# Kernel optimization log

Hardware: AMD Instinct MI355X
Metric: run time of the kernel (lower is better)

The kernel has to match this reference:

```python
import jax, jax.numpy as jnp
import numpy as np

KS = 3   # kernel_size
PAD = 1  # padding
N_K = KS * KS


def conv2d(x, w, b=None, stride=1, pad=0):
    out = jax.lax.conv_general_dilated(
        x, w, (stride, stride), [(pad, pad), (pad, pad)],
        dimension_numbers=('NCHW', 'OIHW', 'NCHW'))
    if b is not None:
        out = out + b[None, :, None, None]
    return out


def deform_sample(x, offset):
    # x: [b,c,H,W]  offset: [b,2N,h,w] -> [b,c,h,w,N]
    b, c, H, W = x.shape
    _, twoN, h, w = offset.shape
    N = twoN // 2
    xp = jnp.pad(x, ((0, 0), (0, 0), (PAD, PAD), (PAD, PAD)))
    Hp, Wp = H + 2 * PAD, W + 2 * PAD
    r = (KS - 1) // 2
    knx, kny = jnp.meshgrid(jnp.arange(-r, r + 1), jnp.arange(-r, r + 1), indexing='ij')
    pnx = knx.reshape(-1).astype(offset.dtype)  # [N] kernel x offsets
    pny = kny.reshape(-1).astype(offset.dtype)
    off = jnp.transpose(offset, (0, 2, 3, 1))   # [b,h,w,2N]
    p0x = (jnp.arange(h) + PAD).astype(offset.dtype)
    p0y = (jnp.arange(w) + PAD).astype(offset.dtype)
    px = p0x[None, :, None, None] + pnx[None, None, None, :] + off[..., :N]  # [b,h,w,N]
    py = p0y[None, None, :, None] + pny[None, None, None, :] + off[..., N:]
    # q = p.detach().floor() in torch -> stop_gradient here
    flx = jnp.floor(jax.lax.stop_gradient(px))
    fly = jnp.floor(jax.lax.stop_gradient(py))
    qltx = jnp.clip(flx, 0, Hp - 1)
    qrbx = jnp.clip(flx + 1, 0, Hp - 1)
    qlty = jnp.clip(fly, 0, Wp - 1)
    qrby = jnp.clip(fly + 1, 0, Wp - 1)
    pxc = jnp.clip(px, 0, Hp - 1)
    pyc = jnp.clip(py, 0, Wp - 1)
    g_lt = (1 + (qltx - pxc)) * (1 + (qlty - pyc))
    g_rb = (1 - (qrbx - pxc)) * (1 - (qrby - pyc))
    g_lb = (1 - (qrbx - pxc)) * (1 + (qlty - pyc))
    g_rt = (1 + (qltx - pxc)) * (1 - (qrby - pyc))
    ix_lt, ix_rb = qltx.astype(jnp.int32), qrbx.astype(jnp.int32)
    iy_lt, iy_rb = qlty.astype(jnp.int32), qrby.astype(jnp.int32)

    def gather(ix, iy):
        def one(xb, ixb, iyb):
            return xb[:, ixb, iyb]  # [c,h,w,N]
        return jax.vmap(one)(xp, ix, iy)

    x_lt = gather(ix_lt, iy_lt)
    x_rb = gather(ix_rb, iy_rb)
    x_lb = gather(ix_rb, iy_lt)
    x_rt = gather(ix_lt, iy_rb)
    return (g_lt[:, None] * x_lt + g_rb[:, None] * x_rb
            + g_lb[:, None] * x_lb + g_rt[:, None] * x_rt)


def z_weight(z, mode):
    # cubic interpolation basis weights; z: [b,N,h,w] -> [b,1,h,w,N]
    if mode == '1':
        w = 1 - 11.0 / 6.0 * z + z ** 2 - 1.0 / 6.0 * z ** 3
    elif mode == '2':
        w = 3 * z - 2.5 * z ** 2 + 0.5 * z ** 3
    elif mode == '4':
        w = -1.5 * z + 2 * z ** 2 - 0.5 * z ** 3
    else:
        w = 1.0 / 3.0 * z - 0.5 * z ** 2 + 1.0 / 6.0 * z ** 3
    return jnp.transpose(w, (0, 2, 3, 1))[:, None]


def reshape_x_offset(xo):
    # [b,c,h,w,ks*ks] -> [b,c,h*ks,w*ks] (torch cat/view equivalent)
    b, c, h, w, _ = xo.shape
    xo = xo.reshape(b, c, h, w, KS, KS)          # N = g*ks + k
    xo = jnp.transpose(xo, (0, 1, 2, 4, 3, 5))   # (b,c,h,g,w,k)
    return xo.reshape(b, c, h * KS, w * KS)


def setup_inputs() -> dict:
    key = jax.random.key(0)
    ks = jax.random.split(key, 18)
    B, C, OSC, OUTC, H, W = 2, 64, 64, 64, 128, 128
    f = jax.random.normal
    inp = {
        'img1': f(ks[0], (B, C, H, W), jnp.float32),
        'img2': f(ks[1], (B, C, H, W), jnp.float32),
        'img4': f(ks[2], (B, C, H, W), jnp.float32),
        'img5': f(ks[3], (B, C, H, W), jnp.float32),
        'offset_source': f(ks[4], (B, OSC, H, W), jnp.float32),
        'w_pc1': f(ks[5], (2 * N_K, OSC, 5, 5), jnp.float32) * 0.01,
        'b_pc1': f(ks[6], (2 * N_K,), jnp.float32) * 0.01,
        'w_pc2': f(ks[7], (2 * N_K, OSC, 5, 5), jnp.float32) * 0.01,
        'b_pc2': f(ks[8], (2 * N_K,), jnp.float32) * 0.01,
        'w_pc4': f(ks[9], (2 * N_K, OSC, 5, 5), jnp.float32) * 0.01,
        'b_pc4': f(ks[10], (2 * N_K,), jnp.float32) * 0.01,
        'w_pc5': f(ks[11], (2 * N_K, OSC, 5, 5), jnp.float32) * 0.01,
        'b_pc5': f(ks[12], (2 * N_K,), jnp.float32) * 0.01,
        'w_z': f(ks[13], (N_K, OSC, 5, 5), jnp.float32) * 0.01,
        'b_z': f(ks[14], (N_K,), jnp.float32) * 0.01,
        'w_m': f(ks[15], (N_K, OSC, 5, 5), jnp.float32) * 0.01,
        'b_m': f(ks[16], (N_K,), jnp.float32) * 0.01,
        'w_conv': f(ks[17], (OUTC, C, KS, KS), jnp.float32) * 0.05,
    }
    return inp


def reference(img1, img2, img4, img5, offset_source,
              w_pc1, b_pc1, w_pc2, b_pc2, w_pc4, b_pc4, w_pc5, b_pc5,
              w_z, b_z, w_m, b_m, w_conv):
    off1 = conv2d(offset_source, w_pc1, b_pc1, pad=2)
    off2 = conv2d(offset_source, w_pc2, b_pc2, pad=2)
    off4 = conv2d(offset_source, w_pc4, b_pc4, pad=2)
    off5 = conv2d(offset_source, w_pc5, b_pc5, pad=2)
    z = 3.0 * jax.nn.sigmoid(conv2d(offset_source, w_z, b_z, pad=2))
    m = jax.nn.sigmoid(conv2d(offset_source, w_m, b_m, pad=2))
    f1 = deform_sample(img1, off1)
    f2 = deform_sample(img2, off2)
    f4 = deform_sample(img4, off4)
    f5 = deform_sample(img5, off5)
    central = (f1 * z_weight(z, '1') + f2 * z_weight(z, '2')
               + f4 * z_weight(z, '4') + f5 * z_weight(z, '5'))
    central = central * jnp.transpose(m, (0, 2, 3, 1))[:, None]
    out = conv2d(reshape_x_offset(central), w_conv, None, stride=KS)
    return out
```

## Files before the change

kernel.cpp:

```cpp
#include <hip/hip_runtime.h>
#include <hip/hip_bf16.h>
#include <math.h>

#define HWX 16384

typedef __attribute__((ext_vector_type(8))) short short8v;
typedef __attribute__((ext_vector_type(4))) float f32x4;

__device__ inline ushort f2bf(float x) {
    union { __hip_bfloat16 h; ushort u; } cv;
    cv.h = __float2bfloat16(x);
    return cv.u;
}

__global__ __launch_bounds__(256) void packw_kernel(
    const float* __restrict__ w1, const float* __restrict__ b1,
    const float* __restrict__ w2, const float* __restrict__ b2,
    const float* __restrict__ w4, const float* __restrict__ b4,
    const float* __restrict__ w5, const float* __restrict__ b5,
    const float* __restrict__ wz, const float* __restrict__ bz,
    const float* __restrict__ wm, const float* __restrict__ bm,
    __hip_bfloat16* __restrict__ Wpk, float* __restrict__ bpack)
{
    const int idx = blockIdx.x * 256 + threadIdx.x;
    if (idx < 96) {
        const int o = idx; float v = 0.f;
        if      (o < 18) v = b1[o];
        else if (o < 36) v = b2[o - 18];
        else if (o < 54) v = b4[o - 36];
        else if (o < 72) v = b5[o - 54];
        else if (o < 81) v = bz[o - 72];
        else if (o < 90) v = bm[o - 81];
        bpack[o] = v;
    }
    if (idx < 96 * 1600) {
        const int o   = idx / 1600;
        const int k   = idx - o * 1600;
        const int kyx = k >> 6;
        const int ic  = k & 63;
        const int off = ic * 25 + kyx;
        float v = 0.f;
        if      (o < 18) v = w1[o * 1600 + off];
        else if (o < 36) v = w2[(o - 18) * 1600 + off];
        else if (o < 54) v = w4[(o - 36) * 1600 + off];
        else if (o < 72) v = w5[(o - 54) * 1600 + off];
        else if (o < 81) v = wz[(o - 72) * 1600 + off];
        else if (o < 90) v = wm[(o - 81) * 1600 + off];
        Wpk[idx] = __float2bfloat16(v);
    }
}

__global__ __launch_bounds__(256) void packosT_kernel(
    const float* __restrict__ src, __hip_bfloat16* __restrict__ osT)
{
    const int yy = blockIdx.x;
    const int b  = blockIdx.y;
    __hip_bfloat16* dst = osT + ((size_t)b * 132 + yy) * 132 * 64;
    for (int idx = threadIdx.x; idx < 132 * 64; idx += 256) {
        const int xx = idx >> 6;
        const int c  = idx & 63;
        float v = 0.f;
        if (yy >= 2 && yy < 130 && xx >= 2 && xx < 130)
            v = src[(((b << 6) + c) << 14) + ((yy - 2) << 7) + (xx - 2)];
        dst[idx] = __float2bfloat16(v);
    }
}

__global__ __launch_bounds__(256) void conv_mfma_kernel(
    const __hip_bfloat16* __restrict__ Wpk,
    const float* __restrict__ bpack,
    const __hip_bfloat16* __restrict__ osT,
    float* __restrict__ offs,
    float* __restrict__ zbuf,
    float* __restrict__ mbuf)
{
    __shared__ __align__(16) ushort slab[5 * 68 * 64];
    __shared__ __align__(16) ushort wbuf[2][96 * 64];

    const int bx = blockIdx.x;
    const int y  = bx >> 1;
    const int x0 = (bx & 1) << 6;
    const int b  = blockIdx.y;
    const int t    = threadIdx.x;
    const int wv   = t >> 6;
    const int lane = t & 63;
    const int l15  = lane & 15;
    const int kgrp = lane >> 4;
    const int wm   = wv >> 1;
    const int wn   = wv & 1;

    const ushort* ob = (const ushort*)osT + (size_t)b * (132 * 132 * 64);
    const ushort* Wg = (const ushort*)Wpk;

    for (int c = t; c < 2720; c += 256) {
        const int r5  = c / 544;
        const int rem = c - r5 * 544;
        const int col = rem >> 3;
        const int cb  = rem & 7;
        const short8v v = *(const short8v*)(ob + (((y + r5) * 132 + x0 + col) << 6) + (cb << 3));
        const int slot = r5 * 544 + (col << 3) + (cb ^ (col & 7));
        *(short8v*)((char*)slab + slot * 16) = v;
    }

#define STAGE_W(kyx, bi)                                                       \
    _Pragma("unroll")                                                          \
    for (int it = 0; it < 3; ++it) {                                           \
        const int c  = it * 256 + t;                                           \
        const int oc = c >> 3, cb = c & 7;                                     \
        const ushort* src = Wg + oc * 1600 + (kyx) * 64 + ((cb ^ (oc & 7)) << 3); \
        __builtin_amdgcn_global_load_lds(                                      \
            (const __attribute__((address_space(1))) void*)src,                \
            (__attribute__((address_space(3))) void*)((char*)wbuf[bi] + (it * 256 + wv * 64) * 16), \
            16, 0, 0);                                                         \
    }

    STAGE_W(0, 0)
    __syncthreads();

    f32x4 acc[3][2];
    #pragma unroll
    for (int m = 0; m < 3; ++m)
        #pragma unroll
        for (int n = 0; n < 2; ++n) acc[m][n] = (f32x4){0.f, 0.f, 0.f, 0.f};

    for (int kyx = 0; kyx < 25; ++kyx) {
        const int bi = kyx & 1;
        if (kyx < 24) STAGE_W(kyx + 1, bi ^ 1)
        const int ky = kyx / 5, kx = kyx % 5;
        #pragma unroll
        for (int kc = 0; kc < 2; ++kc) {
            const int kcg = (kc << 2) + kgrp;
            short8v af[3], bf[2];
            #pragma unroll
            for (int m = 0; m < 3; ++m) {
                const int oc = wm * 48 + m * 16 + l15;
                af[m] = *(const short8v*)((char*)wbuf[bi] + ((oc << 3) + (kcg ^ (oc & 7))) * 16);
            }
            #pragma unroll
            for (int n = 0; n < 2; ++n) {
                const int col = wn * 32 + n * 16 + l15 + kx;
                bf[n] = *(const short8v*)((char*)slab + ((ky * 68 + col) * 8 + (kcg ^ (col & 7))) * 16);
            }
            #pragma unroll
            for (int m = 0; m < 3; ++m)
                #pragma unroll
                for (int n = 0; n < 2; ++n)
                    acc[m][n] = __builtin_amdgcn_mfma_f32_16x16x32_bf16(af[m], bf[n], acc[m][n], 0, 0, 0);
        }
        __syncthreads();
    }
#undef STAGE_W

    #pragma unroll
    for (int m = 0; m < 3; ++m) {
        const int ocb = wm * 48 + m * 16 + (kgrp << 2);
        #pragma unroll
        for (int n = 0; n < 2; ++n) {
            const int x = x0 + wn * 32 + n * 16 + l15;
            const int p = (y << 7) + x;
            #pragma unroll
            for (int r = 0; r < 4; ++r) {
                const int o = ocb + r;
                const float v = acc[m][n][r] + bpack[o];
                if (o < 72) {
                    const int i = o / 18, ch = o - i * 18;
                    offs[i * (2 * 18 * HWX) + (((b * 18) + ch) << 14) + p] = v;
                } else if (o < 81) {
                    zbuf[((b * 9 + (o - 72)) << 14) + p] = 3.f / (1.f + expf(-v));
                } else if (o < 90) {
                    mbuf[((b * 9 + (o - 81)) << 14) + p] = 1.f / (1.f + expf(-v));
                }
            }
        }
    }
}

__global__ __launch_bounds__(256) void transpose_kernel(
    const float* __restrict__ i0, const float* __restrict__ i1,
    const float* __restrict__ i2, const float* __restrict__ i3,
    ushort* __restrict__ imgT)
{
    const int img = blockIdx.z;
    const int b   = blockIdx.y;
    const int p0  = blockIdx.x << 6;
    const float* src = (img == 0) ? i0 : (img == 1) ? i1 : (img == 2) ? i2 : i3;

    __shared__ float tile[64][65];
    const int t = threadIdx.x;
    const int pp = t & 63, c0 = t >> 6;
    #pragma unroll
    for (int k = 0; k < 16; ++k) {
        const int c = (k << 2) + c0;
        tile[c][pp] = src[(((b << 6) + c) << 14) + p0 + pp];
    }
    __syncthreads();
    const int c2 = t & 31, pl = t >> 5;
    #pragma unroll
    for (int k = 0; k < 8; ++k) {
        const int pi = (k << 3) + pl;
        const uint packed = (uint)f2bf(tile[2 * c2][pi])
                          | ((uint)f2bf(tile[2 * c2 + 1][pi]) << 16);
        *(uint*)(imgT + ((size_t)(((img << 1) + b) << 14) + p0 + pi) * 64 + 2 * c2)
            = packed;
    }
}

__global__ __launch_bounds__(256) void wcpk_kernel(
    const float* __restrict__ wc, __hip_bfloat16* __restrict__ WcPk)
{
    const int idx = blockIdx.x * 256 + threadIdx.x;
    if (idx < 36864) WcPk[idx] = __float2bfloat16(wc[idx]);
}

__global__ __launch_bounds__(256, 5) void fused_kernel(
    const float* __restrict__ offs,
    const float* __restrict__ zbuf,
    const float* __restrict__ mbuf,
    const ushort* __restrict__ imgT,
    const __hip_bfloat16* __restrict__ WcPk,
    float* __restrict__ out)
{
    __shared__ __hip_bfloat16 s_sb[16 * 584];
    __shared__ ushort4 s_ti[16 * 36];
    __shared__ float4  s_tw4[16 * 36];

    const int t   = threadIdx.x;
    const int pid = blockIdx.x;
    const int b   = pid >> 10;
    const int rem = pid & 1023;
    const int h   = rem >> 3;
    const int w0p = (rem & 7) << 4;

    for (int u = t; u < 576; u += 256) {
        const int px   = u / 36;
        const int unit = u - px * 36;
        const int i    = unit / 9;
        const int n    = unit - i * 9;
        const int wcol = w0p + px;
        const int p    = (h << 7) + wcol;

        const float* ob = offs + i * (2 * 18 * HWX) + ((b * 18) << 14);
        const float ox = ob[(n << 14) + p];
        const float oy = ob[((n + 9) << 14) + p];
        const float z  = zbuf[((b * 9 + n) << 14) + p];
        const float mm = mbuf[((b * 9 + n) << 14) + p];

        const float zc0 = (i == 0) ? 1.f : 0.f;
        const float zc1 = (i == 0) ? (-11.f / 6.f) : (i == 1) ? 3.f
                         : (i == 2) ? -1.5f : (1.f / 3.f);
        const float zc2 = (i == 0) ? 1.f : (i == 1) ? -2.5f
                         : (i == 2) ? 2.f : -0.5f;
        const float zc3 = (i == 0) ? (-1.f / 6.f) : (i == 1) ? 0.5f
                         : (i == 2) ? -0.5f : (1.f / 6.f);
        const float zw   = zc0 + z * (zc1 + z * (zc2 + z * zc3));
        const float coef = zw * mm;

        const float pxf = (float)(h + n / 3) + ox;
        const float pyf = (float)(wcol + n % 3) + oy;
        const float flx = floorf(pxf), fly = floorf(pyf);
        const float qltx = fminf(fmaxf(flx, 0.f), 129.f);
        const float qrbx = fminf(fmaxf(flx + 1.f, 0.f), 129.f);
        const float qlty = fminf(fmaxf(fly, 0.f), 129.f);
        const float qrby = fminf(fmaxf(fly + 1.f, 0.f), 129.f);
        const float pxc = fminf(fmaxf(pxf, 0.f), 129.f);
        const float pyc = fminf(fmaxf(pyf, 0.f), 129.f);
        const float gxl = 1.f + (qltx - pxc);
        const float gxr = 1.f - (qrbx - pxc);
        const float gyl = 1.f + (qlty - pyc);
        const float gyr = 1.f - (qrby - pyc);
        const int ixl = (int)qltx, ixr = (int)qrbx;
        const int iyl = (int)qlty, iyr = (int)qrby;

        ushort4 ti; float4 tw;
        auto mk = [&](int qx, int qy, float g, ushort& ii, float& ww) {
            const bool valid = (qx >= 1) && (qx <= 128) && (qy >= 1) && (qy <= 128);
            ii = (ushort)(valid ? (((qx - 1) << 7) + (qy - 1)) : 0);
            ww = valid ? g * coef : 0.f;
        };
        mk(ixl, iyl, gxl * gyl, ti.x, tw.x);
        mk(ixr, iyr, gxr * gyr, ti.y, tw.y);
        mk(ixr, iyl, gxr * gyl, ti.z, tw.z);
        mk(ixl, iyr, gxl * gyr, ti.w, tw.w);
        s_ti[u]  = ti;
        s_tw4[u] = tw;
    }
    __syncthreads();

    const int lane = t & 63;
    const int wv   = t >> 6;
    const int c4   = lane & 15;
    const int pxs  = lane >> 4;
    const int px   = (wv << 2) + pxs;

    f32x4 s4[9];
    #pragma unroll
    for (int n = 0; n < 9; ++n) s4[n] = (f32x4){0.f, 0.f, 0.f, 0.f};

    const int tb = px * 36;
    #pragma unroll 1
    for (int i = 0; i < 4; ++i) {
        const char* ibl = (const char*)(imgT + (((size_t)((i << 1) + b)) << 20)) + (c4 << 3);
        #pragma unroll
        for (int n = 0; n < 9; ++n) {
            const ushort4 tib = s_ti[tb + i * 9 + n];
            const float4  tw  = s_tw4[tb + i * 9 + n];
            {
                const uint2 v = *(const uint2*)(ibl + ((uint)tib.x << 7));
                s4[n].x = fmaf(tw.x, __uint_as_float(v.x << 16),         s4[n].x);
                s4[n].y = fmaf(tw.x, __uint_as_float(v.x & 0xffff0000u), s4[n].y);
                s4[n].z = fmaf(tw.x, __uint_as_float(v.y << 16),         s4[n].z);
                s4[n].w = fmaf(tw.x, __uint_as_float(v.y & 0xffff0000u), s4[n].w);
            }
            {
                const uint2 v = *(const uint2*)(ibl + ((uint)tib.y << 7));
                s4[n].x = fmaf(tw.y, __uint_as_float(v.x << 16),         s4[n].x);
                s4[n].y = fmaf(tw.y, __uint_as_float(v.x & 0xffff0000u), s4[n].y);
                s4[n].z = fmaf(tw.y, __uint_as_float(v.y << 16),         s4[n].z);
                s4[n].w = fmaf(tw.y, __uint_as_float(v.y & 0xffff0000u), s4[n].w);
            }
            {
                const uint2 v = *(const uint2*)(ibl + ((uint)tib.z << 7));
                s4[n].x = fmaf(tw.z, __uint_as_float(v.x << 16),         s4[n].x);
                s4[n].y = fmaf(tw.z, __uint_as_float(v.x & 0xffff0000u), s4[n].y);
                s4[n].z = fmaf(tw.z, __uint_as_float(v.y << 16),         s4[n].z);
                s4[n].w = fmaf(tw.z, __uint_as_float(v.y & 0xffff0000u), s4[n].w);
            }
            {
                const uint2 v = *(const uint2*)(ibl + ((uint)tib.w << 7));
                s4[n].x = fmaf(tw.w, __uint_as_float(v.x << 16),         s4[n].x);
                s4[n].y = fmaf(tw.w, __uint_as_float(v.x & 0xffff0000u), s4[n].y);
                s4[n].z = fmaf(tw.w, __uint_as_float(v.y << 16),         s4[n].z);
                s4[n].w = fmaf(tw.w, __uint_as_float(v.y & 0xffff0000u), s4[n].w);
            }
        }
    }

    uint bufu[18];
    #pragma unroll
    for (int k = 0; k < 18; ++k) {
        const int u0 = 2 * k, u1 = 2 * k + 1;
        const float v0 = s4[u0 % 9][u0 / 9];
        const float v1 = s4[u1 % 9][u1 / 9];
        bufu[k] = (uint)f2bf(v0) | ((uint)f2bf(v1) << 16);
    }
    {
        uint2* dst = (uint2*)((char*)s_sb + px * 1168 + c4 * 72);
        #pragma unroll
        for (int k = 0; k < 9; ++k)
            dst[k] = ((const uint2*)bufu)[k];
    }
    __syncthreads();

    const int l15  = lane & 15;
    const int kgrp = lane >> 4;
    const ushort* Wb = (const ushort*)WcPk + (wv * 16 + l15) * 576 + kgrp * 8;
    const ushort* sb = (const ushort*)s_sb + l15 * 584 + kgrp * 8;

    f32x4 acc = {0.f, 0.f, 0.f, 0.f};
    #pragma unroll
    for (int ks = 0; ks < 18; ++ks) {
        const short8v a  = *(const short8v*)(Wb + ks * 32);
        const short8v bb = *(const short8v*)(sb + ks * 32);
        acc = __builtin_amdgcn_mfma_f32_16x16x32_bf16(a, bb, acc, 0, 0, 0);
    }

    const int p = (h << 7) + w0p + l15;
    #pragma unroll
    for (int r = 0; r < 4; ++r) {
        const int oc = wv * 16 + (kgrp << 2) + r;
        out[(((b << 6) + oc) << 14) + p] = acc[r];
    }
}

extern "C" void kernel_launch(void* const* d_in, const int* in_sizes, int n_in,
                              void* d_out, int out_size, void* d_ws, size_t ws_size,
                              hipStream_t stream) {
    (void)in_sizes; (void)n_in; (void)out_size; (void)ws_size;
    const float* img1  = (const float*)d_in[0];
    const float* img2  = (const float*)d_in[1];
    const float* img4  = (const float*)d_in[2];
    const float* img5  = (const float*)d_in[3];
    const float* osrc  = (const float*)d_in[4];
    const float* w_pc1 = (const float*)d_in[5];
    const float* b_pc1 = (const float*)d_in[6];
    const float* w_pc2 = (const float*)d_in[7];
    const float* b_pc2 = (const float*)d_in[8];
    const float* w_pc4 = (const float*)d_in[9];
    const float* b_pc4 = (const float*)d_in[10];
    const float* w_pc5 = (const float*)d_in[11];
    const float* b_pc5 = (const float*)d_in[12];
    const float* w_z   = (const float*)d_in[13];
    const float* b_z   = (const float*)d_in[14];
    const float* w_m   = (const float*)d_in[15];
    const float* b_m   = (const float*)d_in[16];
    const float* w_cv  = (const float*)d_in[17];
    float* out = (float*)d_out;

    float* wsf  = (float*)d_ws;
    float* offs = wsf;
    float* zbuf = wsf + 4 * 589824;
    float* mbuf = zbuf + 294912;
    float* WcTr = mbuf + 294912;
    float* imgTr = WcTr + 36864;

    __hip_bfloat16* WcPk  = (__hip_bfloat16*)WcTr;
    ushort*         imgTb = (ushort*)imgTr;

    __hip_bfloat16* Wpk   = (__hip_bfloat16*)imgTr;
    float*          bpack = imgTr + 76800;
    __hip_bfloat16* osT   = (__hip_bfloat16*)(imgTr + 76912);

    packw_kernel<<<dim3((96 * 1600 + 255) / 256), 256, 0, stream>>>(
        w_pc1, b_pc1, w_pc2, b_pc2, w_pc4, b_pc4, w_pc5, b_pc5,
        w_z, b_z, w_m, b_m, Wpk, bpack);
    packosT_kernel<<<dim3(132, 2), 256, 0, stream>>>(osrc, osT);
    conv_mfma_kernel<<<dim3(256, 2), 256, 0, stream>>>(
        Wpk, bpack, osT, offs, zbuf, mbuf);
    transpose_kernel<<<dim3(256, 2, 4), 256, 0, stream>>>(img1, img2, img4, img5, imgTb);
    wcpk_kernel<<<dim3(144), 256, 0, stream>>>(w_cv, WcPk);
    fused_kernel<<<dim3(2048), 256, 0, stream>>>(offs, zbuf, mbuf, imgTb, WcPk, out);
}
```

Baseline: 118.4 us.

## Restructure deformable gather into 16-byte loads with corner-split lanes and shuffle reduction

Each lane now gathers 8 bf16 channels with a uint4 load instead of 4 channels with a uint2 load. The four bilinear corners are split across two lane halves, whose partial sums are combined with a shuffle-xor. The accumulation loop is reordered to run over kernel taps on the outside, and the s_sb staging layout becomes tap-major; the conv weight pack is permuted to match. Tap indices and weights are packed into one uint4 with bf16 weights, which halves shared memory for tap data and cuts register pressure, at some precision cost in the interpolation weights.

```diff
diff --git a/kernel.cpp b/kernel.cpp
--- a/kernel.cpp
+++ b/kernel.cpp
@@ -70,9 +70,7 @@
     const __hip_bfloat16* __restrict__ Wpk,
     const float* __restrict__ bpack,
     const __hip_bfloat16* __restrict__ osT,
-    float* __restrict__ offs,
-    float* __restrict__ zbuf,
-    float* __restrict__ mbuf)
+    float* __restrict__ offs, float* __restrict__ zbuf, float* __restrict__ mbuf)
 {
     __shared__ __align__(16) ushort slab[5 * 68 * 64];
     __shared__ __align__(16) ushort wbuf[2][96 * 64];
@@ -209,7 +207,13 @@
     const float* __restrict__ wc, __hip_bfloat16* __restrict__ WcPk)
 {
     const int idx = blockIdx.x * 256 + threadIdx.x;
-    if (idx < 36864) WcPk[idx] = __float2bfloat16(wc[idx]);
+    if (idx < 36864) {
+        const int oc  = idx / 576;
+        const int cnp = idx - oc * 576;
+        const int n   = cnp >> 6;
+        const int c   = cnp & 63;
+        WcPk[idx] = __float2bfloat16(wc[oc * 576 + c * 9 + n]);
+    }
 }
 
 __global__ __launch_bounds__(256, 5) void fused_kernel(
@@ -221,8 +225,7 @@
     float* __restrict__ out)
 {
     __shared__ __hip_bfloat16 s_sb[16 * 584];
-    __shared__ ushort4 s_ti[16 * 36];
-    __shared__ float4  s_tw4[16 * 36];
+    __shared__ uint4 s_tap[16 * 36];
 
     const int t   = threadIdx.x;
     const int pid = blockIdx.x;
@@ -232,11 +235,11 @@
     const int w0p = (rem & 7) << 4;
 
     for (int u = t; u < 576; u += 256) {
-        const int px   = u / 36;
-        const int unit = u - px * 36;
+        const int px_  = u / 36;
+        const int unit = u - px_ * 36;
         const int i    = unit / 9;
         const int n    = unit - i * 9;
-        const int wcol = w0p + px;
+        const int wcol = w0p + px_;
         const int p    = (h << 7) + wcol;
 
         const float* ob = offs + i * (2 * 18 * HWX) + ((b * 18) << 14);
@@ -271,83 +274,83 @@
         const int ixl = (int)qltx, ixr = (int)qrbx;
         const int iyl = (int)qlty, iyr = (int)qrby;
 
-        ushort4 ti; float4 tw;
-        auto mk = [&](int qx, int qy, float g, ushort& ii, float& ww) {
+        uint i0_, i1_, i2_, i3_, u0_, u1_, u2_, u3_;
+        auto mk = [&](int qx, int qy, float g, uint& ii, uint& ww) {
             const bool valid = (qx >= 1) && (qx <= 128) && (qy >= 1) && (qy <= 128);
-            ii = (ushort)(valid ? (((qx - 1) << 7) + (qy - 1)) : 0);
-            ww = valid ? g * coef : 0.f;
+            ii = valid ? (uint)(((qx - 1) << 7) + (qy - 1)) : 0u;
+            ww = valid ? (uint)f2bf(g * coef) : 0u;
         };
-        mk(ixl, iyl, gxl * gyl, ti.x, tw.x);
-        mk(ixr, iyr, gxr * gyr, ti.y, tw.y);
-        mk(ixr, iyl, gxr * gyl, ti.z, tw.z);
-        mk(ixl, iyr, gxl * gyr, ti.w, tw.w);
-        s_ti[u]  = ti;
-        s_tw4[u] = tw;
+        mk(ixl, iyl, gxl * gyl, i0_, u0_);
+        mk(ixr, iyr, gxr * gyr, i1_, u1_);
+        mk(ixr, iyl, gxr * gyl, i2_, u2_);
+        mk(ixl, iyr, gxl * gyr, i3_, u3_);
+        uint4 tp;
+        tp.x = i0_ | (i1_ << 16);
+        tp.y = i2_ | (i3_ << 16);
+        tp.z = u0_ | (u1_ << 16);
+        tp.w = u2_ | (u3_ << 16);
+        s_tap[u] = tp;
     }
     __syncthreads();
 
     const int lane = t & 63;
     const int wv   = t >> 6;
-    const int c4   = lane & 15;
+    const int c8   = lane & 7;
+    const int half = (lane >> 3) & 1;
     const int pxs  = lane >> 4;
     const int px   = (wv << 2) + pxs;
-
-    f32x4 s4[9];
-    #pragma unroll
-    for (int n = 0; n < 9; ++n) s4[n] = (f32x4){0.f, 0.f, 0.f, 0.f};
-
-    const int tb = px * 36;
+    const int tb   = px * 36;
+    const int cByte = c8 << 4;
+
     #pragma unroll 1
-    for (int i = 0; i < 4; ++i) {
-        const char* ibl = (const char*)(imgT + (((size_t)((i << 1) + b)) << 20)) + (c4 << 3);
-        #pragma unroll
-        for (int n = 0; n < 9; ++n) {
-            const ushort4 tib = s_ti[tb + i * 9 + n];
-            const float4  tw  = s_tw4[tb + i * 9 + n];
+    for (int n = 0; n < 9; ++n) {
+        float s8[8];
+        #pragma unroll
+        for (int m = 0; m < 8; ++m) s8[m] = 0.f;
+
+        #pragma unroll
+        for (int i = 0; i < 4; ++i) {
+            const uint4 tp = s_tap[tb + i * 9 + n];
+            const uint  pair = half ? tp.y : tp.x;
+            const uint  wpr  = half ? tp.w : tp.z;
+            const float wA = __uint_as_float(wpr << 16);
+            const float wB = __uint_as_float(wpr & 0xffff0000u);
+            const char* ibl = (const char*)imgT + (((size_t)((i << 1) + b)) << 21) + cByte;
             {
-                const uint2 v = *(const uint2*)(ibl + ((uint)tib.x << 7));
-                s4[n].x = fmaf(tw.x, __uint_as_float(v.x << 16),         s4[n].x);
-                s4[n].y = fmaf(tw.x, __uint_as_float(v.x & 0xffff0000u), s4[n].y);
-                s4[n].z = fmaf(tw.x, __uint_as_float(v.y << 16),         s4[n].z);
-                s4[n].w = fmaf(tw.x, __uint_as_float(v.y & 0xffff0000u), s4[n].w);
+                const uint4 v = *(const uint4*)(ibl + ((pair & 0xffffu) << 7));
+                s8[0] = fmaf(wA, __uint_as_float(v.x << 16),         s8[0]);
+                s8[1] = fmaf(wA, __uint_as_float(v.x & 0xffff0000u), s8[1]);
+                s8[2] = fmaf(wA, __uint_as_float(v.y << 16),         s8[2]);
+                s8[3] = fmaf(wA, __uint_as_float(v.y & 0xffff0000u), s8[3]);
+                s8[4] = fmaf(wA, __uint_as_float(v.z << 16),         s8[4]);
+                s8[5] = fmaf(wA, __uint_as_float(v.z & 0xffff0000u), s8[5]);
+                s8[6] = fmaf(wA, __uint_as_float(v.w << 16),         s8[6]);
+                s8[7] = fmaf(wA, __uint_as_float(v.w & 0xffff0000u), s8[7]);
             }
             {
-                const uint2 v = *(const uint2*)(ibl + ((uint)tib.y << 7));
-                s4[n].x = fmaf(tw.y, __uint_as_float(v.x << 16),         s4[n].x);
-                s4[n].y = fmaf(tw.y, __uint_as_float(v.x & 0xffff0000u), s4[n].y);
-                s4[n].z = fmaf(tw.y, __uint_as_float(v.y << 16),         s4[n].z);
-                s4[n].w = fmaf(tw.y, __uint_as_float(v.y & 0xffff0000u), s4[n].w);
-            }
-            {
-                const uint2 v = *(const uint2*)(ibl + ((uint)tib.z << 7));
-                s4[n].x = fmaf(tw.z, __uint_as_float(v.x << 16),         s4[n].x);
-                s4[n].y = fmaf(tw.z, __uint_as_float(v.x & 0xffff0000u), s4[n].y);
-                s4[n].z = fmaf(tw.z, __uint_as_float(v.y << 16),         s4[n].z);
-                s4[n].w = fmaf(tw.z, __uint_as_float(v.y & 0xffff0000u), s4[n].w);
-            }
-            {
-                const uint2 v = *(const uint2*)(ibl + ((uint)tib.w << 7));
-                s4[n].x = fmaf(tw.w, __uint_as_float(v.x << 16),         s4[n].x);
-                s4[n].y = fmaf(tw.w, __uint_as_float(v.x & 0xffff0000u), s4[n].y);
-                s4[n].z = fmaf(tw.w, __uint_as_float(v.y << 16),         s4[n].z);
-                s4[n].w = fmaf(tw.w, __uint_as_float(v.y & 0xffff0000u), s4[n].w);
+                const uint4 v = *(const uint4*)(ibl + ((pair >> 16) << 7));
+                s8[0] = fmaf(wB, __uint_as_float(v.x << 16),         s8[0]);
+                s8[1] = fmaf(wB, __uint_as_float(v.x & 0xffff0000u), s8[1]);
+                s8[2] = fmaf(wB, __uint_as_float(v.y << 16),         s8[2]);
+                s8[3] = fmaf(wB, __uint_as_float(v.y & 0xffff0000u), s8[3]);
+                s8[4] = fmaf(wB, __uint_as_float(v.z << 16),         s8[4]);
+                s8[5] = fmaf(wB, __uint_as_float(v.z & 0xffff0000u), s8[5]);
+                s8[6] = fmaf(wB, __uint_as_float(v.w << 16),         s8[6]);
+                s8[7] = fmaf(wB, __uint_as_float(v.w & 0xffff0000u), s8[7]);
             }
         }
-    }
-
-    uint bufu[18];
-    #pragma unroll
-    for (int k = 0; k < 18; ++k) {
-        const int u0 = 2 * k, u1 = 2 * k + 1;
-        const float v0 = s4[u0 % 9][u0 / 9];
-        const float v1 = s4[u1 % 9][u1 / 9];
-        bufu[k] = (uint)f2bf(v0) | ((uint)f2bf(v1) << 16);
-    }
-    {
-        uint2* dst = (uint2*)((char*)s_sb + px * 1168 + c4 * 72);
-        #pragma unroll
-        for (int k = 0; k < 9; ++k)
-            dst[k] = ((const uint2*)bufu)[k];
+
+        #pragma unroll
+        for (int m = 0; m < 8; ++m) s8[m] += __shfl_xor(s8[m], 8);
+
+        if (half == 0) {
+            uint4 pk;
+            pk.x = (uint)f2bf(s8[0]) | ((uint)f2bf(s8[1]) << 16);
+            pk.y = (uint)f2bf(s8[2]) | ((uint)f2bf(s8[3]) << 16);
+            pk.z = (uint)f2bf(s8[4]) | ((uint)f2bf(s8[5]) << 16);
+            pk.w = (uint)f2bf(s8[6]) | ((uint)f2bf(s8[7]) << 16);
+            *(uint4*)((char*)s_sb + px * 1168 + n * 128 + cByte) = pk;
+        }
     }
     __syncthreads();
 
```

Measured after the change: 104.5 us. -11.7%, faster.
